# Kernel optimization log

Hardware: AMD Instinct MI355X
Metric: run time of the kernel (lower is better)

The kernel has to match this reference:

```python
import jax, jax.numpy as jnp
import numpy as np

N_NODES = 100000
N_EDGES = 1600000
N_GRAPHS = 512
HIDDEN = 128
N_CLASSES = 10


def setup_inputs() -> dict:
    key = jax.random.key(0)
    ks = jax.random.split(key, 12)
    edge_index = jax.random.randint(ks[0], (2, N_EDGES), 0, N_NODES, dtype=jnp.int32)
    batch = jnp.sort(jax.random.randint(ks[1], (N_NODES,), 0, N_GRAPHS, dtype=jnp.int32))
    def lin(k, fi, fo):
        return jax.random.normal(k, (fi, fo), jnp.float32) * (1.0 / np.sqrt(fi))
    return {
        "edge_index": edge_index,
        "batch": batch,
        "W0": lin(ks[2], 1, HIDDEN),
        "b0": jax.random.normal(ks[3], (HIDDEN,), jnp.float32) * 0.01,
        "W1": lin(ks[4], HIDDEN, HIDDEN),
        "b1": jax.random.normal(ks[5], (HIDDEN,), jnp.float32) * 0.01,
        "W2": lin(ks[6], HIDDEN, HIDDEN),
        "b2": jax.random.normal(ks[7], (HIDDEN,), jnp.float32) * 0.01,
        "Wp": lin(ks[8], HIDDEN, N_CLASSES),
        "bp": jax.random.normal(ks[9], (N_CLASSES,), jnp.float32) * 0.01,
    }


def _gcn_setup(edge_index, n_nodes):
    # add self-loops (PyG GCNConv default) and compute symmetric normalization
    loop = jnp.arange(n_nodes, dtype=edge_index.dtype)
    src = jnp.concatenate([edge_index[0], loop])  # [E+N]
    dst = jnp.concatenate([edge_index[1], loop])
    deg = jax.ops.segment_sum(jnp.ones_like(src, dtype=jnp.float32), dst,
                              num_segments=n_nodes)
    dinv = jnp.where(deg > 0, jax.lax.rsqrt(deg), 0.0)
    norm = dinv[src] * dinv[dst]  # [E+N]
    return src, dst, norm


def _gcn_conv(x, W, b, src, dst, norm, n_nodes):
    h = x @ W                                # [N, out]
    msg = h[src] * norm[:, None]             # gather + scale, [E+N, out]
    out = jax.ops.segment_sum(msg, dst, num_segments=n_nodes)
    return out + b


def reference(edge_index, batch, W0, b0, W1, b1, W2, b2, Wp, bp):
    n = batch.shape[0]
    src, dst, norm = _gcn_setup(edge_index, n)
    x = jnp.ones((n, 1), jnp.float32)  # forward() hardcodes ones as features
    for W, b in ((W0, b0), (W1, b1), (W2, b2)):
        x = jax.nn.relu(_gcn_conv(x, W, b, src, dst, norm, n))
        # dropout_p = 0.0 -> identity
    # scatter_mean pooling over graphs
    s = jax.ops.segment_sum(x, batch, num_segments=N_GRAPHS)
    cnt = jax.ops.segment_sum(jnp.ones((n,), jnp.float32), batch,
                              num_segments=N_GRAPHS)
    pooled = s / jnp.maximum(cnt, 1.0)[:, None]
    logits = pooled @ Wp + bp
    return jax.nn.log_softmax(logits, axis=1)
```

## Files before the change

### kernel.cpp

```cpp
#include <hip/hip_runtime.h>

#define HID 128
#define NG 512
#define NC 10
#define BSH 9
#define BSZ (1 << BSH)
#define TILE 4096

typedef unsigned int u32;
typedef unsigned short u16;
typedef __attribute__((ext_vector_type(8))) short short8;
typedef __attribute__((ext_vector_type(4))) float f32x4;

static __device__ __forceinline__ int gtid() {
    return blockIdx.x * blockDim.x + threadIdx.x;
}

static __device__ __forceinline__ u16 f2bf(float f) {
    u32 u = __float_as_uint(f);
    u32 r = u + 0x7fffu + ((u >> 16) & 1u);
    return (u16)(r >> 16);
}
static __device__ __forceinline__ float bf2f(u32 s) {
    return __uint_as_float(s << 16);
}
static __device__ __forceinline__ void bf8_unpack(uint4 u, float* f) {
    f[0] = bf2f(u.x & 0xffffu); f[1] = bf2f(u.x >> 16);
    f[2] = bf2f(u.y & 0xffffu); f[3] = bf2f(u.y >> 16);
    f[4] = bf2f(u.z & 0xffffu); f[5] = bf2f(u.z >> 16);
    f[6] = bf2f(u.w & 0xffffu); f[7] = bf2f(u.w >> 16);
}

__global__ __launch_bounds__(256) void k_bhist(const int* __restrict__ dst,
                                               int* __restrict__ bcnt, int E, int NB) {
    __shared__ int cnt[256];
    int t = threadIdx.x;
    int e0 = blockIdx.x * TILE;
    for (int i = t; i < NB; i += 256) cnt[i] = 0;
    __syncthreads();
#pragma unroll
    for (int k = 0; k < 16; ++k) {
        int e = e0 + k * 256 + t;
        if (e < E) atomicAdd(&cnt[dst[e] >> BSH], 1);
    }
    __syncthreads();
    for (int i = t; i < NB; i += 256)
        if (cnt[i] > 0) atomicAdd(&bcnt[i], cnt[i]);
}

__global__ __launch_bounds__(256) void k_bscan(const int* __restrict__ bcnt,
                                               int* __restrict__ bbase,
                                               int* __restrict__ bcur, int NB, int E) {
    __shared__ int s[256];
    int t = threadIdx.x;
    int own = (t < NB) ? bcnt[t] : 0;
    s[t] = own;
    __syncthreads();
    for (int off = 1; off < 256; off <<= 1) {
        int v = (t >= off) ? s[t - off] : 0;
        __syncthreads();
        s[t] += v;
        __syncthreads();
    }
    if (t < NB) {
        int b = s[t] - own;
        bbase[t] = b;
        bcur[t] = b;
    }
    if (t == 0) bbase[NB] = E;
}

__global__ __launch_bounds__(256) void k_part1(const int* __restrict__ src,
                                               const int* __restrict__ dst,
                                               int* __restrict__ bcur,
                                               uint2* __restrict__ tmp, int E, int NB) {
    __shared__ int cnt[256];
    __shared__ int base[256];
    int t = threadIdx.x;
    int e0 = blockIdx.x * TILE;
    for (int i = t; i < NB; i += 256) cnt[i] = 0;
    __syncthreads();
    int s_[16], d_[16];
#pragma unroll
    for (int k = 0; k < 16; ++k) {
        int e = e0 + k * 256 + t;
        if (e < E) {
            s_[k] = src[e];
            d_[k] = dst[e];
            atomicAdd(&cnt[d_[k] >> BSH], 1);
        } else {
            d_[k] = -1;
        }
    }
    __syncthreads();
    for (int i = t; i < NB; i += 256) {
        if (cnt[i] > 0) base[i] = atomicAdd(&bcur[i], cnt[i]);
        cnt[i] = 0;
    }
    __syncthreads();
#pragma unroll
    for (int k = 0; k < 16; ++k) {
        if (d_[k] >= 0) {
            int b = d_[k] >> BSH;
            int pos = base[b] + atomicAdd(&cnt[b], 1);
            tmp[pos] = make_uint2((u32)s_[k], (u32)d_[k]);
        }
    }
}

__global__ __launch_bounds__(512) void k_part2(const int* __restrict__ bbase,
                                               const uint2* __restrict__ tmp,
                                               u32* __restrict__ packed,
                                               int* __restrict__ rowptr,
                                               float* __restrict__ dinv,
                                               int N, int NB) {
    __shared__ int cnt[BSZ];
    __shared__ int scn[BSZ];
    __shared__ int cur[BSZ];
    int b = blockIdx.x;
    int v0 = b << BSH;
    int nv = N - v0; if (nv > BSZ) nv = BSZ;
    int t = threadIdx.x;
    int e0 = bbase[b], e1 = bbase[b + 1];

    cnt[t] = 0;
    __syncthreads();
    for (int e = e0 + t; e < e1; e += 512)
        atomicAdd(&cnt[tmp[e].y & (BSZ - 1)], 1);
    __syncthreads();
    int own = cnt[t];
    scn[t] = own;
    __syncthreads();
    for (int off = 1; off < BSZ; off <<= 1) {
        int v = (t >= off) ? scn[t - off] : 0;
        __syncthreads();
        scn[t] += v;
        __syncthreads();
    }
    int start = e0 + scn[t] - own;
    cur[t] = start;
    if (t < nv) {
        rowptr[v0 + t] = start;
        dinv[v0 + t] = rsqrtf(1.0f + (float)own);
    }
    if (b == NB - 1 && t == 0) rowptr[N] = e1;
    __syncthreads();
    for (int e = e0 + t; e < e1; e += 512) {
        uint2 p = tmp[e];
        int pos = atomicAdd(&cur[p.y & (BSZ - 1)], 1);
        packed[pos] = p.x;
    }
}

__global__ __launch_bounds__(256) void k_sl0(const int* __restrict__ rowptr,
                                             const u32* __restrict__ packed,
                                             const float* __restrict__ dinv,
                                             const float* __restrict__ W0,
                                             const float* __restrict__ b0,
                                             u16* __restrict__ x, int N) {
    int lane = threadIdx.x & 31;
    int v = (blockIdx.x * 256 + threadIdx.x) >> 5;
    if (v >= N) return;
    int r0 = rowptr[v], r1 = rowptr[v + 1];
    float s = 0.0f;
    for (int j = r0 + lane; j < r1; j += 32) s += dinv[packed[j]];
#pragma unroll
    for (int off = 16; off > 0; off >>= 1) s += __shfl_xor(s, off, 32);
    float di = dinv[v];
    s = di * (di + s);
    int d0 = lane * 4;
    float4 w = *(const float4*)&W0[d0];
    float4 b = *(const float4*)&b0[d0];
    float a0 = fmaxf(fmaf(s, w.x, b.x), 0.0f);
    float a1 = fmaxf(fmaf(s, w.y, b.y), 0.0f);
    float a2 = fmaxf(fmaf(s, w.z, b.z), 0.0f);
    float a3 = fmaxf(fmaf(s, w.w, b.w), 0.0f);
    uint2 o;
    o.x = (u32)f2bf(a0) | ((u32)f2bf(a1) << 16);
    o.y = (u32)f2bf(a2) | ((u32)f2bf(a3) << 16);
    *(uint2*)&x[(size_t)v * HID + d0] = o;
}

__global__ __launch_bounds__(256) void k_wt(const float* __restrict__ W,
                                            u16* __restrict__ Wt) {
    int t = gtid();
    if (t >= 2048) return;
    int n = t >> 4;
    int j = t & 15;
    int js = j ^ (n & 7);
    u32 w0 = (u32)f2bf(W[(j * 8 + 0) * HID + n]) | ((u32)f2bf(W[(j * 8 + 1) * HID + n]) << 16);
    u32 w1 = (u32)f2bf(W[(j * 8 + 2) * HID + n]) | ((u32)f2bf(W[(j * 8 + 3) * HID + n]) << 16);
    u32 w2 = (u32)f2bf(W[(j * 8 + 4) * HID + n]) | ((u32)f2bf(W[(j * 8 + 5) * HID + n]) << 16);
    u32 w3 = (u32)f2bf(W[(j * 8 + 6) * HID + n]) | ((u32)f2bf(W[(j * 8 + 7) * HID + n]) << 16);
    uint4 o = make_uint4(w0, w1, w2, w3);
    *(uint4*)&Wt[(size_t)n * HID + js * 8] = o;
}

__global__ __launch_bounds__(256) void k_gemm(const u16* __restrict__ x,
                                              const u16* __restrict__ Wt,
                                              const float* __restrict__ dinv,
                                              u16* __restrict__ q, int nrows) {
    __shared__ u16 Wl[HID * HID];
    int tid = threadIdx.x;
    for (int i = tid; i < 2048; i += 256)
        *(uint4*)&Wl[i * 8] = *(const uint4*)&Wt[i * 8];

    int w = tid >> 6;
    int l = tid & 63;
    int R0 = blockIdx.x * 64 + w * 16;
    int arow = R0 + (l & 15);
    int koff = (l >> 4) * 8;

    short8 a[4];
#pragma unroll
    for (int kb = 0; kb < 4; ++kb) {
        if (arow < nrows)
            a[kb] = *(const short8*)&x[(size_t)arow * HID + kb * 32 + koff];
        else
            a[kb] = (short8)0;
    }
    __syncthreads();

    int colbase = l & 15;
    int rowq = (l >> 4) * 4;
    float dv[4];
#pragma unroll
    for (int i = 0; i < 4; ++i) {
        int orow = R0 + rowq + i;
        dv[i] = (orow < nrows) ? dinv[orow] : 0.0f;
    }
#pragma unroll
    for (int cb = 0; cb < 8; ++cb) {
        f32x4 acc = {0.0f, 0.0f, 0.0f, 0.0f};
        int wrow = cb * 16 + (l & 15);
#pragma unroll
        for (int kb = 0; kb < 4; ++kb) {
            int j = (kb * 4 + (l >> 4)) ^ (wrow & 7);
            short8 b = *(const short8*)&Wl[wrow * HID + j * 8];
            acc = __builtin_amdgcn_mfma_f32_16x16x32_bf16(a[kb], b, acc, 0, 0, 0);
        }
#pragma unroll
        for (int i = 0; i < 4; ++i) {
            int orow = R0 + rowq + i;
            if (orow < nrows)
                q[(size_t)orow * HID + cb * 16 + colbase] = f2bf(acc[i] * dv[i]);
        }
    }
}

__global__ __launch_bounds__(256) void k_aggr(const u32* __restrict__ packed,
                                              const int* __restrict__ rowptr,
                                              const u16* __restrict__ q,
                                              const float* __restrict__ dinv,
                                              const float* __restrict__ b,
                                              u16* __restrict__ y, int N) {
    int lane = threadIdx.x & 31;
    int v = (blockIdx.x * 256 + threadIdx.x) >> 5;
    if (v >= N) return;
    int r0 = rowptr[v], r1 = rowptr[v + 1];
    int half = lane >> 4;
    int d8 = (lane & 15) * 8;

    float acc[8];
    if (half == 0) {
        uint4 qv = *(const uint4*)&q[(size_t)v * HID + d8];
        bf8_unpack(qv, acc);
    } else {
#pragma unroll
        for (int j = 0; j < 8; ++j) acc[j] = 0.0f;
    }

    for (int base = r0; base < r1; base += 32) {
        int idx = base + lane;
        u32 e = (idx < r1) ? packed[idx] : 0xFFFFFFFFu;
        int m = r1 - base; if (m > 32) m = 32;
        int iters = (m + 1) >> 1;
        for (int k = 0; k < iters; ++k) {
            u32 s = __shfl(e, 2 * k + half, 32);
            if (s != 0xFFFFFFFFu) {
                uint4 hq = *(const uint4*)&q[(size_t)s * HID + d8];
                float f[8];
                bf8_unpack(hq, f);
#pragma unroll
                for (int j = 0; j < 8; ++j) acc[j] += f[j];
            }
        }
    }
#pragma unroll
    for (int j = 0; j < 8; ++j) acc[j] += __shfl_xor(acc[j], 16, 32);

    if (half == 0) {
        float dv = dinv[v];
        float4 b0 = *(const float4*)&b[d8];
        float4 b1 = *(const float4*)&b[d8 + 4];
        float o[8];
        o[0] = fmaxf(fmaf(acc[0], dv, b0.x), 0.0f);
        o[1] = fmaxf(fmaf(acc[1], dv, b0.y), 0.0f);
        o[2] = fmaxf(fmaf(acc[2], dv, b0.z), 0.0f);
        o[3] = fmaxf(fmaf(acc[3], dv, b0.w), 0.0f);
        o[4] = fmaxf(fmaf(acc[4], dv, b1.x), 0.0f);
        o[5] = fmaxf(fmaf(acc[5], dv, b1.y), 0.0f);
        o[6] = fmaxf(fmaf(acc[6], dv, b1.z), 0.0f);
        o[7] = fmaxf(fmaf(acc[7], dv, b1.w), 0.0f);
        uint4 u;
        u.x = (u32)f2bf(o[0]) | ((u32)f2bf(o[1]) << 16);
        u.y = (u32)f2bf(o[2]) | ((u32)f2bf(o[3]) << 16);
        u.z = (u32)f2bf(o[4]) | ((u32)f2bf(o[5]) << 16);
        u.w = (u32)f2bf(o[6]) | ((u32)f2bf(o[7]) << 16);
        *(uint4*)&y[(size_t)v * HID + d8] = u;
    }
}


__global__ void k_pool(const u16* __restrict__ x, const int* __restrict__ batch,
                       float* __restrict__ pooled, float* __restrict__ cnt, int N) {
    const int K = 32;
    int d = threadIdx.x & (HID - 1);
    int chunk = blockIdx.x * 2 + (threadIdx.x >> 7);
    int v0 = chunk * K;
    if (v0 >= N) return;
    int vend = v0 + K; if (vend > N) vend = N;
    int g = batch[v0];
    float acc = 0.0f, c = 0.0f;
    for (int v = v0; v < vend; ++v) {
        int gv = batch[v];
        if (gv != g) {
            atomicAdd(&pooled[g * HID + d], acc);
            if (d == 0) atomicAdd(&cnt[g], c);
            acc = 0.0f; c = 0.0f; g = gv;
        }
        acc += bf2f((u32)x[(size_t)v * HID + d]);
        c += 1.0f;
    }
    atomicAdd(&pooled[g * HID + d], acc);
    if (d == 0) atomicAdd(&cnt[g], c);
}

__global__ void k_head(const float* __restrict__ pooled, const float* __restrict__ cnt,
                       const float* __restrict__ Wp, const float* __restrict__ bp,
                       float* __restrict__ out) {
    int g = gtid();
    if (g >= NG) return;
    float inv = 1.0f / fmaxf(cnt[g], 1.0f);
    float l[NC];
#pragma unroll
    for (int c = 0; c < NC; ++c) l[c] = bp[c];
    for (int d = 0; d < HID; ++d) {
        float pv = pooled[g * HID + d] * inv;
#pragma unroll
        for (int c = 0; c < NC; ++c) l[c] = fmaf(pv, Wp[d * NC + c], l[c]);
    }
    float m = l[0];
#pragma unroll
    for (int c = 1; c < NC; ++c) m = fmaxf(m, l[c]);
    float s = 0.0f;
#pragma unroll
    for (int c = 0; c < NC; ++c) s += expf(l[c] - m);
    float ls = logf(s) + m;
#pragma unroll
    for (int c = 0; c < NC; ++c) out[g * NC + c] = l[c] - ls;
}

extern "C" void kernel_launch(void* const* d_in, const int* in_sizes, int n_in,
                              void* d_out, int out_size, void* d_ws, size_t ws_size,
                              hipStream_t stream) {
    const int* ei    = (const int*)d_in[0];
    int E            = in_sizes[0] / 2;
    const int* src   = ei;
    const int* dstp  = ei + E;
    const int* batch = (const int*)d_in[1];
    int N            = in_sizes[1];
    const float* W0  = (const float*)d_in[2];
    const float* b0  = (const float*)d_in[3];
    const float* W1  = (const float*)d_in[4];
    const float* b1  = (const float*)d_in[5];
    const float* W2  = (const float*)d_in[6];
    const float* b2  = (const float*)d_in[7];
    const float* Wp  = (const float*)d_in[8];
    const float* bp  = (const float*)d_in[9];
    float* out       = (float*)d_out;

    u16*  xA     = (u16*)d_ws;
    u16*  xB     = xA + (size_t)N * HID;
    u32*  packed = (u32*)(xB + (size_t)N * HID);
    uint2* tmp   = (uint2*)(packed + E);
    u16*  Wt1    = (u16*)(tmp + E);
    u16*  Wt2    = Wt1 + HID * HID;
    int*  rowptr = (int*)(Wt2 + HID * HID);
    int*  bcnt   = rowptr + N + 1;
    int*  bbase  = bcnt + 256;
    int*  bcur   = bbase + 257;
    float* dinv  = (float*)(bcur + 256);
    float* pooled= dinv + N;
    float* cntg  = pooled + NG * HID;

    auto cdiv = [](int a, int b) { return (a + b - 1) / b; };
    int NB = cdiv(N, BSZ);

    hipMemsetAsync(bcnt, 0, 256 * sizeof(int), stream);
    hipMemsetAsync(pooled, 0, (NG * HID + NG) * sizeof(float), stream);

    k_bhist<<<cdiv(E, TILE), 256, 0, stream>>>(dstp, bcnt, E, NB);
    k_bscan<<<1, 256, 0, stream>>>(bcnt, bbase, bcur, NB, E);
    k_part1<<<cdiv(E, TILE), 256, 0, stream>>>(src, dstp, bcur, tmp, E, NB);
    k_part2<<<NB, 512, 0, stream>>>(bbase, tmp, packed, rowptr, dinv, N, NB);

    k_wt<<<8, 256, 0, stream>>>(W1, Wt1);
    k_wt<<<8, 256, 0, stream>>>(W2, Wt2);

    k_sl0<<<cdiv(N, 8), 256, 0, stream>>>(rowptr, packed, dinv, W0, b0, xA, N);

    k_gemm<<<cdiv(N, 64), 256, 0, stream>>>(xA, Wt1, dinv, xB, N);
    k_aggr<<<cdiv(N, 8), 256, 0, stream>>>(packed, rowptr, xB, dinv, b1, xA, N);

    k_gemm<<<cdiv(N, 64), 256, 0, stream>>>(xA, Wt2, dinv, xB, N);
    k_aggr<<<cdiv(N, 8), 256, 0, stream>>>(packed, rowptr, xB, dinv, b2, xA, N);

    k_pool<<<cdiv(cdiv(N, 32), 2), 256, 0, stream>>>(xA, batch, pooled, cntg, N);
    k_head<<<2, 256, 0, stream>>>(pooled, cntg, Wp, bp, out);
}
```

Measured before the change: 281.4 us.

## Pack partition entries into 32 bits, unroll aggregation gathers, vectorize pooling

The bucket partition now stores each edge as one 32-bit word (source shifted left plus the low destination bits) instead of an 8-byte pair, which halves the temporary traffic in both partition kernels. The aggregation inner loop handles two neighbor rows per step so more gather loads are in flight at once. Pooling now has each thread read 8 bf16 values with a single vector load across 16-lane groups, which means more chunks per block. Packing assumes source ids fit in 23 bits, and pooling now issues 8 atomics per thread at each graph boundary.

```diff
diff --git a/kernel.cpp b/kernel.cpp
--- a/kernel.cpp
+++ b/kernel.cpp
@@ -6,6 +6,7 @@
 #define BSH 9
 #define BSZ (1 << BSH)
 #define TILE 4096
+#define NOEDGE 0xFFFFFFFFu
 
 typedef unsigned int u32;
 typedef unsigned short u16;
@@ -73,23 +74,25 @@
 __global__ __launch_bounds__(256) void k_part1(const int* __restrict__ src,
                                                const int* __restrict__ dst,
                                                int* __restrict__ bcur,
-                                               uint2* __restrict__ tmp, int E, int NB) {
+                                               u32* __restrict__ tmp, int E, int NB) {
     __shared__ int cnt[256];
     __shared__ int base[256];
     int t = threadIdx.x;
     int e0 = blockIdx.x * TILE;
     for (int i = t; i < NB; i += 256) cnt[i] = 0;
     __syncthreads();
-    int s_[16], d_[16];
+    u32 p_[16];
+    int b_[16];
 #pragma unroll
     for (int k = 0; k < 16; ++k) {
         int e = e0 + k * 256 + t;
         if (e < E) {
-            s_[k] = src[e];
-            d_[k] = dst[e];
-            atomicAdd(&cnt[d_[k] >> BSH], 1);
+            int d = dst[e];
+            p_[k] = ((u32)src[e] << BSH) | (u32)(d & (BSZ - 1));
+            b_[k] = d >> BSH;
+            atomicAdd(&cnt[b_[k]], 1);
         } else {
-            d_[k] = -1;
+            b_[k] = -1;
         }
     }
     __syncthreads();
@@ -100,16 +103,15 @@
     __syncthreads();
 #pragma unroll
     for (int k = 0; k < 16; ++k) {
-        if (d_[k] >= 0) {
-            int b = d_[k] >> BSH;
-            int pos = base[b] + atomicAdd(&cnt[b], 1);
-            tmp[pos] = make_uint2((u32)s_[k], (u32)d_[k]);
+        if (b_[k] >= 0) {
+            int pos = base[b_[k]] + atomicAdd(&cnt[b_[k]], 1);
+            tmp[pos] = p_[k];
         }
     }
 }
 
 __global__ __launch_bounds__(512) void k_part2(const int* __restrict__ bbase,
-                                               const uint2* __restrict__ tmp,
+                                               const u32* __restrict__ tmp,
                                                u32* __restrict__ packed,
                                                int* __restrict__ rowptr,
                                                float* __restrict__ dinv,
@@ -126,7 +128,7 @@
     cnt[t] = 0;
     __syncthreads();
     for (int e = e0 + t; e < e1; e += 512)
-        atomicAdd(&cnt[tmp[e].y & (BSZ - 1)], 1);
+        atomicAdd(&cnt[tmp[e] & (BSZ - 1)], 1);
     __syncthreads();
     int own = cnt[t];
     scn[t] = own;
@@ -146,9 +148,9 @@
     if (b == NB - 1 && t == 0) rowptr[N] = e1;
     __syncthreads();
     for (int e = e0 + t; e < e1; e += 512) {
-        uint2 p = tmp[e];
-        int pos = atomicAdd(&cur[p.y & (BSZ - 1)], 1);
-        packed[pos] = p.x;
+        u32 p = tmp[e];
+        int pos = atomicAdd(&cur[p & (BSZ - 1)], 1);
+        packed[pos] = p >> BSH;
     }
 }
 
@@ -272,17 +274,31 @@
 
     for (int base = r0; base < r1; base += 32) {
         int idx = base + lane;
-        u32 e = (idx < r1) ? packed[idx] : 0xFFFFFFFFu;
+        u32 e = (idx < r1) ? packed[idx] : NOEDGE;
         int m = r1 - base; if (m > 32) m = 32;
         int iters = (m + 1) >> 1;
-        for (int k = 0; k < iters; ++k) {
-            u32 s = __shfl(e, 2 * k + half, 32);
-            if (s != 0xFFFFFFFFu) {
-                uint4 hq = *(const uint4*)&q[(size_t)s * HID + d8];
-                float f[8];
-                bf8_unpack(hq, f);
-#pragma unroll
-                for (int j = 0; j < 8; ++j) acc[j] += f[j];
+        int k = 0;
+        for (; k + 2 <= iters; k += 2) {
+            u32 s0 = __shfl(e, 2 * k + half, 32);
+            u32 s1 = __shfl(e, 2 * k + 2 + half, 32);
+            uint4 h0 = make_uint4(0, 0, 0, 0);
+            uint4 h1 = make_uint4(0, 0, 0, 0);
+            if (s0 != NOEDGE) h0 = *(const uint4*)&q[(size_t)s0 * HID + d8];
+            if (s1 != NOEDGE) h1 = *(const uint4*)&q[(size_t)s1 * HID + d8];
+            float f0[8], f1[8];
+            bf8_unpack(h0, f0);
+            bf8_unpack(h1, f1);
+#pragma unroll
+            for (int j = 0; j < 8; ++j) acc[j] += f0[j] + f1[j];
+        }
+        if (k < iters) {
+            u32 s0 = __shfl(e, 2 * k + half, 32);
+            if (s0 != NOEDGE) {
+                uint4 h0 = *(const uint4*)&q[(size_t)s0 * HID + d8];
+                float f0[8];
+                bf8_unpack(h0, f0);
+#pragma unroll
+                for (int j = 0; j < 8; ++j) acc[j] += f0[j];
             }
         }
     }
@@ -311,29 +327,41 @@
     }
 }
 
-
-__global__ void k_pool(const u16* __restrict__ x, const int* __restrict__ batch,
-                       float* __restrict__ pooled, float* __restrict__ cnt, int N) {
+__global__ __launch_bounds__(256) void k_pool(const u16* __restrict__ x,
+                                              const int* __restrict__ batch,
+                                              float* __restrict__ pooled,
+                                              float* __restrict__ cntg, int N) {
     const int K = 32;
-    int d = threadIdx.x & (HID - 1);
-    int chunk = blockIdx.x * 2 + (threadIdx.x >> 7);
+    int grp = threadIdx.x >> 4;
+    int lane16 = threadIdx.x & 15;
+    int d8 = lane16 * 8;
+    int chunk = blockIdx.x * 16 + grp;
     int v0 = chunk * K;
     if (v0 >= N) return;
     int vend = v0 + K; if (vend > N) vend = N;
     int g = batch[v0];
-    float acc = 0.0f, c = 0.0f;
+    float acc[8] = {0, 0, 0, 0, 0, 0, 0, 0};
+    float c = 0.0f;
     for (int v = v0; v < vend; ++v) {
         int gv = batch[v];
         if (gv != g) {
-            atomicAdd(&pooled[g * HID + d], acc);
-            if (d == 0) atomicAdd(&cnt[g], c);
-            acc = 0.0f; c = 0.0f; g = gv;
-        }
-        acc += bf2f((u32)x[(size_t)v * HID + d]);
+#pragma unroll
+            for (int j = 0; j < 8; ++j) atomicAdd(&pooled[g * HID + d8 + j], acc[j]);
+            if (lane16 == 0) atomicAdd(&cntg[g], c);
+#pragma unroll
+            for (int j = 0; j < 8; ++j) acc[j] = 0.0f;
+            c = 0.0f; g = gv;
+        }
+        uint4 u = *(const uint4*)&x[(size_t)v * HID + d8];
+        float f[8];
+        bf8_unpack(u, f);
+#pragma unroll
+        for (int j = 0; j < 8; ++j) acc[j] += f[j];
         c += 1.0f;
     }
-    atomicAdd(&pooled[g * HID + d], acc);
-    if (d == 0) atomicAdd(&cnt[g], c);
+#pragma unroll
+    for (int j = 0; j < 8; ++j) atomicAdd(&pooled[g * HID + d8 + j], acc[j]);
+    if (lane16 == 0) atomicAdd(&cntg[g], c);
 }
 
 __global__ void k_head(const float* __restrict__ pooled, const float* __restrict__ cnt,
@@ -383,7 +411,7 @@
     u16*  xA     = (u16*)d_ws;
     u16*  xB     = xA + (size_t)N * HID;
     u32*  packed = (u32*)(xB + (size_t)N * HID);
-    uint2* tmp   = (uint2*)(packed + E);
+    u32*  tmp    = packed + E;
     u16*  Wt1    = (u16*)(tmp + E);
     u16*  Wt2    = Wt1 + HID * HID;
     int*  rowptr = (int*)(Wt2 + HID * HID);
@@ -416,6 +444,6 @@
     k_gemm<<<cdiv(N, 64), 256, 0, stream>>>(xA, Wt2, dinv, xB, N);
     k_aggr<<<cdiv(N, 8), 256, 0, stream>>>(packed, rowptr, xB, dinv, b2, xA, N);
 
-    k_pool<<<cdiv(cdiv(N, 32), 2), 256, 0, stream>>>(xA, batch, pooled, cntg, N);
+    k_pool<<<cdiv(cdiv(N, 32), 16), 256, 0, stream>>>(xA, batch, pooled, cntg, N);
     k_head<<<2, 256, 0, stream>>>(pooled, cntg, Wp, bp, out);
 }
```

After: 292.6 us. 1.04x slower.
